# Optimization experiments

Measured on AMD Instinct MI355X. Metric: run time of the kernel, lower is better.

## Reference

```python
import jax, jax.numpy as jnp
import numpy as np

IMAGE_SIZE = (256, 704)
VOXEL_SIZE = (0.5, 0.5, 1.5)
N_VOXELS = (200, 200, 4)
VOXEL_CENTER = (0.0, 0.0, -1.7)
BN_EPS = 1e-5
B, N_CAM, C_IN, HF, WF, C_OUT = 2, 6, 256, 32, 88, 80


def _get_points():
    nx, ny, nz = N_VOXELS
    pts = jnp.stack(jnp.meshgrid(jnp.arange(nx), jnp.arange(ny), jnp.arange(nz), indexing='ij')).astype(jnp.float32)
    vs = jnp.asarray(VOXEL_SIZE, jnp.float32)
    origin = jnp.asarray(VOXEL_CENTER, jnp.float32) - jnp.asarray(N_VOXELS, jnp.float32) / 2.0 * vs
    pts = pts * vs.reshape(3, 1, 1, 1) + origin.reshape(3, 1, 1, 1)
    return pts.reshape(3, -1)  # [3, N], N = nx*ny*nz


def setup_inputs():
    key = jax.random.key(0)
    k0, k1 = jax.random.split(key)
    mlvl_feats = jax.random.normal(k0, (B, N_CAM, C_IN, HF, WF), jnp.float32)
    # realistic lidar2image = intrinsics @ extrinsics for 6 surround cameras
    H, W = IMAGE_SIZE
    K = np.eye(4, dtype=np.float32)
    K[0, 0], K[1, 1], K[0, 2], K[1, 2] = 350.0, 350.0, W / 2.0, H / 2.0
    l2i = np.zeros((B, N_CAM, 4, 4), np.float32)
    A = np.array([[0, -1, 0], [0, 0, -1], [1, 0, 0]], np.float32)  # lidar->camera axis remap
    for j in range(N_CAM):
        yaw = 2.0 * np.pi * j / N_CAM
        cz, sz = np.cos(yaw), np.sin(yaw)
        Rz = np.array([[cz, -sz, 0], [sz, cz, 0], [0, 0, 1]], np.float32)
        R = A @ Rz.T
        t = Rz @ np.array([1.0, 0.0, 1.5], np.float32)  # camera position in lidar frame
        E = np.eye(4, dtype=np.float32)
        E[:3, :3] = R
        E[:3, 3] = -R @ t
        l2i[:, j] = K @ E
    lidar2image = jnp.asarray(l2i)
    img_aug_matrix = jnp.tile(jnp.eye(4, dtype=jnp.float32), (B, N_CAM, 1, 1))
    lidar_aug_matrix = jnp.tile(jnp.eye(4, dtype=jnp.float32), (B, 1, 1))
    conv_w = jax.random.normal(k1, (C_OUT, C_IN), jnp.float32) * 0.05
    conv_b = jnp.zeros((C_OUT,), jnp.float32)
    bn_gamma = jnp.ones((C_OUT,), jnp.float32)
    bn_beta = jnp.zeros((C_OUT,), jnp.float32)
    bn_mean = jnp.zeros((C_OUT,), jnp.float32)
    bn_var = jnp.ones((C_OUT,), jnp.float32)
    return {"mlvl_feats": mlvl_feats, "lidar2image": lidar2image, "img_aug_matrix": img_aug_matrix,
            "lidar_aug_matrix": lidar_aug_matrix, "conv_w": conv_w, "conv_b": conv_b,
            "bn_gamma": bn_gamma, "bn_beta": bn_beta, "bn_mean": bn_mean, "bn_var": bn_var}


def _sample_volume(feat, l2i, iam, lam, pts):
    # feat: [n_cam, C, Hf, Wf]; l2i/iam: [n_cam,4,4]; lam: [4,4]; pts: [3,N]
    n_img, C, Hh, Ww = feat.shape
    stride = (IMAGE_SIZE[-1] + Ww - 1) // Ww  # ceil(image_W / feat_W)
    p = pts - lam[:3, 3:4]
    p = lam[:3, :3].T @ p  # inverse lidar aug
    iam_r = iam.at[:, :3, 3].set(0.0)  # img aug with translation zeroed
    proj = (iam_r @ l2i)[:, :3, :]  # [n_cam, 3, 4]
    ph = jnp.concatenate([p, jnp.ones((1, p.shape[1]), p.dtype)], axis=0)  # [4, N]
    p2i = jnp.einsum('nij,jk->nik', proj, ph)  # [n_cam, 3, N]
    Z = p2i[:, 2]
    u = p2i[:, 0] / Z + iam[:, 0, 3][:, None]
    v = p2i[:, 1] / Z + iam[:, 1, 3][:, None]
    u_fm = jnp.round(u / stride).astype(jnp.int32)
    v_fm = jnp.round(v / stride).astype(jnp.int32)
    valid = (u_fm >= 0) & (v_fm >= 0) & (u_fm < Ww) & (v_fm < Hh) & (Z > 0)
    uc = jnp.clip(u_fm, 0, Ww - 1)
    vc = jnp.clip(v_fm, 0, Hh - 1)
    vol = jnp.zeros((C, pts.shape[1]), feat.dtype)
    for j in range(n_img):  # fixed small camera count; later cameras overwrite, matching torch loop
        vol = jnp.where(valid[j][None, :], feat[j][:, vc[j], uc[j]], vol)
    return vol.reshape(C, *N_VOXELS).sum(axis=-1)  # sum over z -> [C, nx, ny]


def reference(mlvl_feats, lidar2image, img_aug_matrix, lidar_aug_matrix, conv_w, conv_b, bn_gamma, bn_beta, bn_mean, bn_var):
    pts = _get_points()
    bev = jax.vmap(_sample_volume, in_axes=(0, 0, 0, 0, None))(
        mlvl_feats, lidar2image, img_aug_matrix, lidar_aug_matrix, pts)  # [B, C, nx, ny]
    out = jnp.einsum('bcxy,oc->boxy', bev, conv_w) + conv_b[None, :, None, None]
    scale = (bn_gamma / jnp.sqrt(bn_var + BN_EPS))[None, :, None, None]
    out = (out - bn_mean[None, :, None, None]) * scale + bn_beta[None, :, None, None]
    return jnp.maximum(out, 0.0)
```

## Files before the change

### kernel.cpp

```cpp
#include <hip/hip_runtime.h>

#define BATCH 2
#define NCAM 6
#define CIN 256
#define COUT 80
#define HFEAT 32
#define WFEAT 88
#define HWF (HFEAT * WFEAT)
#define NXV 200
#define NYV 200
#define NZV 4
#define NPIX (NXV * NYV)
#define BN_EPS 1e-5f
#define CSPLIT 2
#define CHALF (COUT / CSPLIT)

#define WS_NEED ((size_t)BATCH * NCAM * HWF * COUT * 4)

__device__ __forceinline__ void compute_cam_mat(int b, int cam,
                                                const float* __restrict__ l2i,
                                                const float* __restrict__ iam,
                                                const float* __restrict__ lam,
                                                float* __restrict__ O ) {
    const float* L = lam + b * 16;
    const float* A = iam + (b * NCAM + cam) * 16;
    const float* P = l2i + (b * NCAM + cam) * 16;
    float Tl[3][4];
    #pragma unroll
    for (int i = 0; i < 3; i++) {
        #pragma unroll
        for (int j = 0; j < 3; j++) Tl[i][j] = L[j * 4 + i];
        Tl[i][3] = -(L[0 * 4 + i] * L[0 * 4 + 3] +
                     L[1 * 4 + i] * L[1 * 4 + 3] +
                     L[2 * 4 + i] * L[2 * 4 + 3]);
    }
    float Pm[3][4];
    #pragma unroll
    for (int i = 0; i < 3; i++)
        #pragma unroll
        for (int j = 0; j < 4; j++) {
            float s = 0.f;
            #pragma unroll
            for (int k = 0; k < 3; k++) s += A[i * 4 + k] * P[k * 4 + j];
            Pm[i][j] = s;
        }
    #pragma unroll
    for (int i = 0; i < 3; i++) {
        #pragma unroll
        for (int j = 0; j < 4; j++) {
            float s = (j == 3) ? Pm[i][3] : 0.f;
            #pragma unroll
            for (int k = 0; k < 3; k++) s += Pm[i][k] * Tl[k][j];
            O[i * 4 + j] = s;
        }
    }
    O[12] = A[0 * 4 + 3];
    O[13] = A[1 * 4 + 3];
    O[14] = 0.f;
    O[15] = 0.f;
}

__global__ __launch_bounds__(256) void k_featw(const float* __restrict__ feat,
                                               const float* __restrict__ W,
                                               float* __restrict__ featW) {
    const int hw = blockIdx.x * 256 + threadIdx.x;
    const int bc = blockIdx.y;
    const int og = blockIdx.z;
    const float* f = feat + (size_t)bc * CIN * HWF + hw;
    const float* w = W + og * 20 * CIN;
    float acc[20];
    #pragma unroll
    for (int j = 0; j < 20; j++) acc[j] = 0.f;
    #pragma unroll 4
    for (int c = 0; c < CIN; c++) {
        float v = f[(size_t)c * HWF];
        #pragma unroll
        for (int j = 0; j < 20; j++) acc[j] = fmaf(v, w[j * CIN + c], acc[j]);
    }
    float* dst = featW + ((size_t)bc * HWF + hw) * COUT + og * 20;
    #pragma unroll
    for (int j = 0; j < 5; j++) {
        *reinterpret_cast<float4*>(dst + j * 4) =
            make_float4(acc[j * 4], acc[j * 4 + 1], acc[j * 4 + 2], acc[j * 4 + 3]);
    }
}

__device__ __forceinline__ int project_point(const float* __restrict__ M ,
                                             float x, float y, float z) {
    for (int cam = NCAM - 1; cam >= 0; --cam) {
        const float* m = M + cam * 16;
        float Z = m[8] * x + m[9] * y + m[10] * z + m[11];
        if (Z > 0.f) {
            float u = (m[0] * x + m[1] * y + m[2] * z + m[3]) / Z + m[12];
            float v = (m[4] * x + m[5] * y + m[6] * z + m[7]) / Z + m[13];
            float uf = rintf(u * 0.125f);
            float vf = rintf(v * 0.125f);
            if (uf >= 0.f && uf < (float)WFEAT && vf >= 0.f && vf < (float)HFEAT) {
                return cam * HWF + (int)vf * WFEAT + (int)uf;
            }
        }
    }
    return -1;
}

__device__ __forceinline__ void bn_precompute(const float* __restrict__ cb,
                                              const float* __restrict__ gamma,
                                              const float* __restrict__ beta,
                                              const float* __restrict__ mean,
                                              const float* __restrict__ var,
                                              float* __restrict__ s_scale,
                                              float* __restrict__ s_bias) {
    for (int o = threadIdx.x; o < COUT; o += 64) {
        float sc = gamma[o] / sqrtf(var[o] + BN_EPS);
        s_scale[o] = sc;
        s_bias[o] = (cb[o] - mean[o]) * sc + beta[o];
    }
}

__global__ __launch_bounds__(64, 2) void k_bev(const float* __restrict__ featW,
                                               const float* __restrict__ l2i,
                                               const float* __restrict__ iam,
                                               const float* __restrict__ lam,
                                               const float* __restrict__ cb,
                                               const float* __restrict__ gamma,
                                               const float* __restrict__ beta,
                                               const float* __restrict__ mean,
                                               const float* __restrict__ var,
                                               float* __restrict__ out) {
    __shared__ float smats[NCAM * 16];
    __shared__ float s_scale[COUT];
    __shared__ float s_bias[COUT];
    const int b = blockIdx.y;
    const int cs = blockIdx.z;
    if (threadIdx.x < NCAM)
        compute_cam_mat(b, threadIdx.x, l2i, iam, lam, smats + threadIdx.x * 16);
    bn_precompute(cb, gamma, beta, mean, var, s_scale, s_bias);
    __syncthreads();

    const int P = blockIdx.x * 64 + threadIdx.x;
    const int ix = P / NYV, iy = P % NYV;
    const float x = ix * 0.5f - 50.0f;
    const float y = iy * 0.5f - 50.0f;

    const float* base = featW + (size_t)b * NCAM * HWF * COUT + cs * CHALF;
    const float4* src[NZV];
    float vmask[NZV];
    #pragma unroll
    for (int iz = 0; iz < NZV; ++iz) {
        float z = iz * 1.5f - 4.7f;
        int off = project_point(smats, x, y, z);
        vmask[iz] = (off >= 0) ? 1.0f : 0.0f;
        src[iz] = reinterpret_cast<const float4*>(
            base + (size_t)((off >= 0) ? off : 0) * COUT);
    }

    float4 buf[NZV][10];
    #pragma unroll
    for (int iz = 0; iz < NZV; ++iz)
        #pragma unroll
        for (int i = 0; i < 10; i++) buf[iz][i] = src[iz][i];

    float4 acc[10];
    #pragma unroll
    for (int i = 0; i < 10; i++) acc[i] = make_float4(0.f, 0.f, 0.f, 0.f);
    #pragma unroll
    for (int iz = 0; iz < NZV; ++iz) {
        float m = vmask[iz];
        #pragma unroll
        for (int i = 0; i < 10; i++) {
            acc[i].x = fmaf(m, buf[iz][i].x, acc[i].x);
            acc[i].y = fmaf(m, buf[iz][i].y, acc[i].y);
            acc[i].z = fmaf(m, buf[iz][i].z, acc[i].z);
            acc[i].w = fmaf(m, buf[iz][i].w, acc[i].w);
        }
    }

    float* op = out + ((size_t)b * COUT + cs * CHALF) * NPIX + P;
    #pragma unroll
    for (int i = 0; i < 10; i++) {
        float a[4] = {acc[i].x, acc[i].y, acc[i].z, acc[i].w};
        #pragma unroll
        for (int j = 0; j < 4; j++) {
            int o = cs * CHALF + i * 4 + j;
            float val = fmaf(a[j], s_scale[o], s_bias[o]);
            op[(size_t)(i * 4 + j) * NPIX] = fmaxf(val, 0.f);
        }
    }
}

__global__ __launch_bounds__(64) void k_bev_fb(const float* __restrict__ feat,
                                               const float* __restrict__ l2i,
                                               const float* __restrict__ iam,
                                               const float* __restrict__ lam,
                                               const float* __restrict__ W,
                                               const float* __restrict__ cb,
                                               const float* __restrict__ gamma,
                                               const float* __restrict__ beta,
                                               const float* __restrict__ mean,
                                               const float* __restrict__ var,
                                               float* __restrict__ out) {
    __shared__ float smats[NCAM * 16];
    __shared__ float s_scale[COUT];
    __shared__ float s_bias[COUT];
    const int b = blockIdx.y;
    if (threadIdx.x < NCAM)
        compute_cam_mat(b, threadIdx.x, l2i, iam, lam, smats + threadIdx.x * 16);
    bn_precompute(cb, gamma, beta, mean, var, s_scale, s_bias);
    __syncthreads();

    const int P = blockIdx.x * 64 + threadIdx.x;
    const int ix = P / NYV, iy = P % NYV;
    const float x = ix * 0.5f - 50.0f;
    const float y = iy * 0.5f - 50.0f;

    float acc[COUT];
    #pragma unroll
    for (int o = 0; o < COUT; o++) acc[o] = 0.f;

    for (int iz = 0; iz < NZV; ++iz) {
        float z = iz * 1.5f - 4.7f;
        int off = project_point(smats, x, y, z);
        if (off >= 0) {
            const float* fp = feat + (size_t)b * NCAM * CIN * HWF +
                              (size_t)(off / HWF) * CIN * HWF + (off % HWF);
            for (int c = 0; c < CIN; c++) {
                float fv = fp[(size_t)c * HWF];
                #pragma unroll 8
                for (int o = 0; o < COUT; o++) acc[o] = fmaf(fv, W[o * CIN + c], acc[o]);
            }
        }
    }

    float* op = out + (size_t)b * COUT * NPIX + P;
    for (int o = 0; o < COUT; o++) {
        float val = fmaf(acc[o], s_scale[o], s_bias[o]);
        op[(size_t)o * NPIX] = fmaxf(val, 0.f);
    }
}

extern "C" void kernel_launch(void* const* d_in, const int* in_sizes, int n_in,
                              void* d_out, int out_size, void* d_ws, size_t ws_size,
                              hipStream_t stream) {
    const float* feat  = (const float*)d_in[0];
    const float* l2i   = (const float*)d_in[1];
    const float* iam   = (const float*)d_in[2];
    const float* lam   = (const float*)d_in[3];
    const float* W     = (const float*)d_in[4];
    const float* cb    = (const float*)d_in[5];
    const float* gamma = (const float*)d_in[6];
    const float* beta  = (const float*)d_in[7];
    const float* mean  = (const float*)d_in[8];
    const float* var   = (const float*)d_in[9];
    float* out = (float*)d_out;

    if (ws_size >= WS_NEED) {
        float* featW = (float*)d_ws;
        k_featw<<<dim3(11, 12, 4), 256, 0, stream>>>(feat, W, featW);
        k_bev<<<dim3(625, 2, CSPLIT), 64, 0, stream>>>(featW, l2i, iam, lam, cb,
                                                       gamma, beta, mean, var, out);
    } else {
        k_bev_fb<<<dim3(625, 2), 64, 0, stream>>>(feat, l2i, iam, lam, W, cb, gamma,
                                                  beta, mean, var, out);
    }
}
```

Measured before the change: 156.9 us.

## Store projected features as fp16 and stage conv weights in LDS

The intermediate per-pixel projected features (feat·W) are now written as half precision, which halves workspace traffic and the gather bytes read by the BEV kernel. The BEV kernel converts the half2 values back to float before accumulating. The featw kernel moves to 64-thread blocks that load their 20×256 weight slice into shared memory and read it as float4 vectors instead of scalar global loads. This trades some rounding error in the intermediate values for less memory traffic, and also drops the occupancy hint on k_bev.

Result: faster. 140.8 us (-10.2%).

```diff
diff --git a/kernel.cpp b/kernel.cpp
--- a/kernel.cpp
+++ b/kernel.cpp
@@ -1,4 +1,5 @@
 #include <hip/hip_runtime.h>
+#include <hip/hip_fp16.h>
 
 #define BATCH 2
 #define NCAM 6
@@ -15,7 +16,7 @@
 #define CSPLIT 2
 #define CHALF (COUT / CSPLIT)
 
-#define WS_NEED ((size_t)BATCH * NCAM * HWF * COUT * 4)
+#define WS_NEED ((size_t)BATCH * NCAM * HWF * COUT * 2)
 
 __device__ __forceinline__ void compute_cam_mat(int b, int cam,
                                                 const float* __restrict__ l2i,
@@ -60,29 +61,53 @@
     O[15] = 0.f;
 }
 
-__global__ __launch_bounds__(256) void k_featw(const float* __restrict__ feat,
-                                               const float* __restrict__ W,
-                                               float* __restrict__ featW) {
-    const int hw = blockIdx.x * 256 + threadIdx.x;
+__global__ __launch_bounds__(64) void k_featw(const float* __restrict__ feat,
+                                              const float* __restrict__ W,
+                                              __half* __restrict__ featW) {
+    __shared__ __align__(16) float wl[CIN][20];
+    const int l = threadIdx.x;
     const int bc = blockIdx.y;
     const int og = blockIdx.z;
+
+    #pragma unroll
+    for (int j = 0; j < 20; j++) {
+        #pragma unroll
+        for (int q = 0; q < 4; q++) {
+            int c = q * 64 + l;
+            wl[c][j] = W[(og * 20 + j) * CIN + c];
+        }
+    }
+    __syncthreads();
+
+    const int hw = blockIdx.x * 64 + l;
     const float* f = feat + (size_t)bc * CIN * HWF + hw;
-    const float* w = W + og * 20 * CIN;
+
     float acc[20];
     #pragma unroll
     for (int j = 0; j < 20; j++) acc[j] = 0.f;
-    #pragma unroll 4
+
+    #pragma unroll 8
     for (int c = 0; c < CIN; c++) {
         float v = f[(size_t)c * HWF];
-        #pragma unroll
-        for (int j = 0; j < 20; j++) acc[j] = fmaf(v, w[j * CIN + c], acc[j]);
-    }
-    float* dst = featW + ((size_t)bc * HWF + hw) * COUT + og * 20;
-    #pragma unroll
-    for (int j = 0; j < 5; j++) {
-        *reinterpret_cast<float4*>(dst + j * 4) =
-            make_float4(acc[j * 4], acc[j * 4 + 1], acc[j * 4 + 2], acc[j * 4 + 3]);
-    }
+        const float4* wr = reinterpret_cast<const float4*>(&wl[c][0]);
+        float4 w0 = wr[0], w1 = wr[1], w2 = wr[2], w3 = wr[3], w4 = wr[4];
+        acc[0]  = fmaf(v, w0.x, acc[0]);   acc[1]  = fmaf(v, w0.y, acc[1]);
+        acc[2]  = fmaf(v, w0.z, acc[2]);   acc[3]  = fmaf(v, w0.w, acc[3]);
+        acc[4]  = fmaf(v, w1.x, acc[4]);   acc[5]  = fmaf(v, w1.y, acc[5]);
+        acc[6]  = fmaf(v, w1.z, acc[6]);   acc[7]  = fmaf(v, w1.w, acc[7]);
+        acc[8]  = fmaf(v, w2.x, acc[8]);   acc[9]  = fmaf(v, w2.y, acc[9]);
+        acc[10] = fmaf(v, w2.z, acc[10]);  acc[11] = fmaf(v, w2.w, acc[11]);
+        acc[12] = fmaf(v, w3.x, acc[12]);  acc[13] = fmaf(v, w3.y, acc[13]);
+        acc[14] = fmaf(v, w3.z, acc[14]);  acc[15] = fmaf(v, w3.w, acc[15]);
+        acc[16] = fmaf(v, w4.x, acc[16]);  acc[17] = fmaf(v, w4.y, acc[17]);
+        acc[18] = fmaf(v, w4.z, acc[18]);  acc[19] = fmaf(v, w4.w, acc[19]);
+    }
+
+    __half2* dst = reinterpret_cast<__half2*>(
+        featW + ((size_t)bc * HWF + hw) * COUT + og * 20);
+    #pragma unroll
+    for (int j = 0; j < 10; j++)
+        dst[j] = __floats2half2_rn(acc[2 * j], acc[2 * j + 1]);
 }
 
 __device__ __forceinline__ int project_point(const float* __restrict__ M ,
@@ -117,16 +142,16 @@
     }
 }
 
-__global__ __launch_bounds__(64, 2) void k_bev(const float* __restrict__ featW,
-                                               const float* __restrict__ l2i,
-                                               const float* __restrict__ iam,
-                                               const float* __restrict__ lam,
-                                               const float* __restrict__ cb,
-                                               const float* __restrict__ gamma,
-                                               const float* __restrict__ beta,
-                                               const float* __restrict__ mean,
-                                               const float* __restrict__ var,
-                                               float* __restrict__ out) {
+__global__ __launch_bounds__(64) void k_bev(const __half* __restrict__ featW,
+                                            const float* __restrict__ l2i,
+                                            const float* __restrict__ iam,
+                                            const float* __restrict__ lam,
+                                            const float* __restrict__ cb,
+                                            const float* __restrict__ gamma,
+                                            const float* __restrict__ beta,
+                                            const float* __restrict__ mean,
+                                            const float* __restrict__ var,
+                                            float* __restrict__ out) {
     __shared__ float smats[NCAM * 16];
     __shared__ float s_scale[COUT];
     __shared__ float s_bias[COUT];
@@ -142,49 +167,48 @@
     const float x = ix * 0.5f - 50.0f;
     const float y = iy * 0.5f - 50.0f;
 
-    const float* base = featW + (size_t)b * NCAM * HWF * COUT + cs * CHALF;
-    const float4* src[NZV];
+    const __half* base = featW + (size_t)b * NCAM * HWF * COUT + cs * CHALF;
+    const uint4* src[NZV];
     float vmask[NZV];
     #pragma unroll
     for (int iz = 0; iz < NZV; ++iz) {
         float z = iz * 1.5f - 4.7f;
         int off = project_point(smats, x, y, z);
         vmask[iz] = (off >= 0) ? 1.0f : 0.0f;
-        src[iz] = reinterpret_cast<const float4*>(
+        src[iz] = reinterpret_cast<const uint4*>(
             base + (size_t)((off >= 0) ? off : 0) * COUT);
     }
 
-    float4 buf[NZV][10];
+    uint4 buf[NZV][5];
     #pragma unroll
     for (int iz = 0; iz < NZV; ++iz)
         #pragma unroll
-        for (int i = 0; i < 10; i++) buf[iz][i] = src[iz][i];
-
-    float4 acc[10];
-    #pragma unroll
-    for (int i = 0; i < 10; i++) acc[i] = make_float4(0.f, 0.f, 0.f, 0.f);
+        for (int i = 0; i < 5; i++) buf[iz][i] = src[iz][i];
+
+    float acc[CHALF];
+    #pragma unroll
+    for (int k = 0; k < CHALF; k++) acc[k] = 0.f;
     #pragma unroll
     for (int iz = 0; iz < NZV; ++iz) {
         float m = vmask[iz];
         #pragma unroll
-        for (int i = 0; i < 10; i++) {
-            acc[i].x = fmaf(m, buf[iz][i].x, acc[i].x);
-            acc[i].y = fmaf(m, buf[iz][i].y, acc[i].y);
-            acc[i].z = fmaf(m, buf[iz][i].z, acc[i].z);
-            acc[i].w = fmaf(m, buf[iz][i].w, acc[i].w);
+        for (int i = 0; i < 5; i++) {
+            const __half2* h2 = reinterpret_cast<const __half2*>(&buf[iz][i]);
+            #pragma unroll
+            for (int k = 0; k < 4; k++) {
+                float2 fv = __half22float2(h2[k]);
+                acc[i * 8 + k * 2]     = fmaf(m, fv.x, acc[i * 8 + k * 2]);
+                acc[i * 8 + k * 2 + 1] = fmaf(m, fv.y, acc[i * 8 + k * 2 + 1]);
+            }
         }
     }
 
     float* op = out + ((size_t)b * COUT + cs * CHALF) * NPIX + P;
     #pragma unroll
-    for (int i = 0; i < 10; i++) {
-        float a[4] = {acc[i].x, acc[i].y, acc[i].z, acc[i].w};
-        #pragma unroll
-        for (int j = 0; j < 4; j++) {
-            int o = cs * CHALF + i * 4 + j;
-            float val = fmaf(a[j], s_scale[o], s_bias[o]);
-            op[(size_t)(i * 4 + j) * NPIX] = fmaxf(val, 0.f);
-        }
+    for (int k = 0; k < CHALF; k++) {
+        int o = cs * CHALF + k;
+        float val = fmaf(acc[k], s_scale[o], s_bias[o]);
+        op[(size_t)k * NPIX] = fmaxf(val, 0.f);
     }
 }
 
@@ -254,9 +278,9 @@
     float* out = (float*)d_out;
 
     if (ws_size >= WS_NEED) {
-        float* featW = (float*)d_ws;
-        k_featw<<<dim3(11, 12, 4), 256, 0, stream>>>(feat, W, featW);
-        k_bev<<<dim3(625, 2, CSPLIT), 64, 0, stream>>>(featW, l2i, iam, lam, cb,
+        __half* featWp = (__half*)d_ws;
+        k_featw<<<dim3(44, 12, 4), 64, 0, stream>>>(feat, W, featWp);
+        k_bev<<<dim3(625, 2, CSPLIT), 64, 0, stream>>>(featWp, l2i, iam, lam, cb,
                                                        gamma, beta, mean, var, out);
     } else {
         k_bev_fb<<<dim3(625, 2), 64, 0, stream>>>(feat, l2i, iam, lam, W, cb, gamma,
```
